# Optimization experiments

Measured on AMD Instinct MI355X. Metric: run time of the kernel, lower is better.

The kernel has to match this reference:

```python
import jax, jax.numpy as jnp
import numpy as np

H = 768          # hidden_size
NH = 12          # num heads
HD = H // NH     # head dim = 64
FF = 4 * H       # 3072
EPS = 1e-12


def _layer_norm(x, g, b):
    mu = jnp.mean(x, axis=-1, keepdims=True)
    var = jnp.var(x, axis=-1, keepdims=True)
    return (x - mu) * jax.lax.rsqrt(var + EPS) * g + b


def setup_inputs() -> dict:
    key = jax.random.key(0)
    ks = jax.random.split(key, 8)
    B, S = 4, 2048
    s = 0.02
    return {
        "x": jax.random.normal(ks[0], (B, S, H), dtype=jnp.float32),
        "w_qkv": jax.random.normal(ks[1], (H, 3 * H), dtype=jnp.float32) * s,
        "b_qkv": jnp.zeros((3 * H,), dtype=jnp.float32),
        "w_out": jax.random.normal(ks[2], (H, H), dtype=jnp.float32) * s,
        "b_out": jnp.zeros((H,), dtype=jnp.float32),
        "w_ff1": jax.random.normal(ks[3], (H, FF), dtype=jnp.float32) * s,
        "b_ff1": jnp.zeros((FF,), dtype=jnp.float32),
        "w_ff2": jax.random.normal(ks[4], (FF, H), dtype=jnp.float32) * s,
        "b_ff2": jnp.zeros((H,), dtype=jnp.float32),
        "g1": jnp.ones((H,), dtype=jnp.float32),
        "be1": jnp.zeros((H,), dtype=jnp.float32),
        "g2": jnp.ones((H,), dtype=jnp.float32),
        "be2": jnp.zeros((H,), dtype=jnp.float32),
    }


def reference(x, w_qkv, b_qkv, w_out, b_out, w_ff1, b_ff1, w_ff2, b_ff2, g1, be1, g2, be2):
    B, S, _ = x.shape
    qkv = x @ w_qkv + b_qkv                     # [B,S,3H]
    q, k, v = jnp.split(qkv, 3, axis=-1)
    # [B,S,H] -> [B,NH,S,HD]
    def heads(t):
        return t.reshape(B, S, NH, HD).transpose(0, 2, 1, 3)
    q, k, v = heads(q), heads(k), heads(v)
    scores = jnp.einsum("bhqd,bhkd->bhqk", q, k) / np.sqrt(HD).astype(np.float32)
    attn = jax.nn.softmax(scores, axis=-1)      # dropout is identity at inference
    ctx = jnp.einsum("bhqk,bhkd->bhqd", attn, v)
    ctx = ctx.transpose(0, 2, 1, 3).reshape(B, S, H)
    attn_out = ctx @ w_out + b_out
    x1 = _layer_norm(x + attn_out, g1, be1)
    h = jax.nn.gelu(x1 @ w_ff1 + b_ff1, approximate=False)  # torch exact gelu
    ffn = h @ w_ff2 + b_ff2
    return _layer_norm(x1 + ffn, g2, be2)
```

## Files before the change

### kernel.cpp

```cpp
#include <hip/hip_runtime.h>
#include <cstdint>
#include <cstddef>

typedef unsigned short u16;
typedef __attribute__((ext_vector_type(8))) short bf16x8;
typedef __attribute__((ext_vector_type(4))) float f32x4;
typedef __attribute__((ext_vector_type(16))) float f32x16;

__device__ __forceinline__ u16 f2b(float f) {
    union { float f; unsigned u; } un; un.f = f;
    unsigned r = un.u + 0x7fffu + ((un.u >> 16) & 1u);
    return (u16)(r >> 16);
}
__device__ __forceinline__ u16 f2b_trunc(float f) {
    union { float f; unsigned u; } un; un.f = f;
    return (u16)(un.u >> 16);
}
__device__ __forceinline__ float b2f(u16 h) {
    union { unsigned u; float f; } un; un.u = ((unsigned)h) << 16;
    return un.f;
}
__device__ __forceinline__ float fast_exp2(float x) {
#if __has_builtin(__builtin_amdgcn_exp2f)
    return __builtin_amdgcn_exp2f(x);
#else
    return exp2f(x);
#endif
}
__device__ __forceinline__ float fast_rcp(float x) {
#if __has_builtin(__builtin_amdgcn_rcpf)
    return __builtin_amdgcn_rcpf(x);
#else
    return 1.f / x;
#endif
}
__device__ __forceinline__ float gelu_fast(float v) {
    const float s = fast_exp2(v * (2.30220842f + 0.10294324f * (v * v)));
    return v - v * fast_rcp(s + 1.f);
}

__device__ __forceinline__ void stage16(const u16* g, u16* l) {
    __builtin_amdgcn_global_load_lds(
        (const __attribute__((address_space(1))) void*)g,
        (__attribute__((address_space(3))) void*)l, 16, 0, 0);
}

__global__ __launch_bounds__(256)
void prep(const float* __restrict__ x, u16* __restrict__ xb,
          const float* __restrict__ wqkv, u16* __restrict__ wqkvT,
          const float* __restrict__ wout, u16* __restrict__ woutT,
          const float* __restrict__ wff1, u16* __restrict__ wff1T,
          const float* __restrict__ wff2, u16* __restrict__ wff2T) {
    __shared__ float t[32][33];
    const int tid = threadIdx.x;
    int bid = blockIdx.x;
    if (bid < 6144) {
        const int i = bid * 256 + tid;
        float4 v = ((const float4*)x)[i];
        ushort4 o;
        o.x = f2b(v.x); o.y = f2b(v.y); o.z = f2b(v.z); o.w = f2b(v.w);
        ((ushort4*)xb)[i] = o;
        return;
    }
    int tt = bid - 6144;
    const float* in; u16* out; int K, N, bx, by;
    if (tt < 1728)      { in = wqkv; out = wqkvT; K = 768;  N = 2304; bx = tt % 72; by = tt / 72; }
    else if ((tt -= 1728) < 576)  { in = wout; out = woutT; K = 768;  N = 768;  bx = tt % 24; by = tt / 24; }
    else if ((tt -= 576) < 2304)  { in = wff1; out = wff1T; K = 768;  N = 3072; bx = tt % 96; by = tt / 96; }
    else { tt -= 2304;    in = wff2; out = wff2T; K = 3072; N = 768;  bx = tt % 24; by = tt / 24; }
    const int n0 = bx * 32, k0 = by * 32;
    const int tx = tid & 31, ty = tid >> 5;
#pragma unroll
    for (int i = 0; i < 4; ++i)
        t[ty + i * 8][tx] = in[(size_t)(k0 + ty + i * 8) * N + n0 + tx];
    __syncthreads();
#pragma unroll
    for (int i = 0; i < 4; ++i)
        out[(size_t)(n0 + ty + i * 8) * K + k0 + tx] = f2b(t[tx][ty + i * 8]);
}

template <int EPI, int NTW>
__global__ __launch_bounds__(256, 3)
void gemm_bf16(const u16* __restrict__ A, const u16* __restrict__ BT,
               const float* __restrict__ bias,
               void* __restrict__ outp, u16* __restrict__ vt, int M, int N, int K) {
    __shared__ __align__(16) u16 Ash[128 * 64];
    __shared__ __align__(16) u16 Bsh[NTW * 64 * 64];
    const int m0 = blockIdx.y * 128, n0 = blockIdx.x * (NTW * 64);
    const int tid = threadIdx.x;
    const int w = tid >> 6, lane = tid & 63;
    const int l32 = lane & 31, half = lane >> 5;
    const int wm = (w >> 1) * 64, wn = (w & 1) * (NTW * 32);

    const int srow = lane >> 3;
    const int sgrp = (lane & 7) ^ (srow & 7);
    const int xr = l32 & 7;

    f32x16 acc[2][NTW];
#pragma unroll
    for (int i = 0; i < 2; ++i)
#pragma unroll
        for (int j = 0; j < NTW; ++j)
#pragma unroll
            for (int e = 0; e < 16; ++e) acc[i][j][e] = 0.f;

    for (int k0 = 0; k0 < K; k0 += 64) {
#pragma unroll
        for (int it = 0; it < 4; ++it) {
            const int c = it * 4 + w;
            const int r = c * 8 + srow;
            stage16(A + (size_t)(m0 + r) * K + k0 + sgrp * 8, &Ash[c * 512 + lane * 8]);
        }
#pragma unroll
        for (int it = 0; it < 2 * NTW; ++it) {
            const int c = it * 4 + w;
            const int r = c * 8 + srow;
            stage16(BT + (size_t)(n0 + r) * K + k0 + sgrp * 8, &Bsh[c * 512 + lane * 8]);
        }
        __syncthreads();

        if constexpr (NTW == 2) {
            bf16x8 af[2][4], bfr[2][4];
#pragma unroll
            for (int mt = 0; mt < 2; ++mt)
#pragma unroll
                for (int kc = 0; kc < 4; ++kc)
                    af[mt][kc] = *(const bf16x8*)&Ash[(wm + mt * 32 + l32) * 64 +
                                                      (((kc << 1) + half) ^ xr) * 8];
#pragma unroll
            for (int nt = 0; nt < 2; ++nt)
#pragma unroll
                for (int kc = 0; kc < 4; ++kc)
                    bfr[nt][kc] = *(const bf16x8*)&Bsh[(wn + nt * 32 + l32) * 64 +
                                                       (((kc << 1) + half) ^ xr) * 8];
#pragma unroll
            for (int mt = 0; mt < 2; ++mt)
#pragma unroll
                for (int nt = 0; nt < 2; ++nt)
#pragma unroll
                    for (int kc = 0; kc < 4; ++kc)
                        acc[mt][nt] = __builtin_amdgcn_mfma_f32_32x32x16_bf16(
                            af[mt][kc], bfr[nt][kc], acc[mt][nt], 0, 0, 0);
        } else {
#pragma unroll
            for (int kc = 0; kc < 4; ++kc) {
                const int ko = (((kc << 1) + half) ^ xr) * 8;
                bf16x8 a0 = *(const bf16x8*)&Ash[(wm + l32) * 64 + ko];
                bf16x8 a1 = *(const bf16x8*)&Ash[(wm + 32 + l32) * 64 + ko];
#pragma unroll
                for (int nt = 0; nt < NTW; ++nt) {
                    bf16x8 bv = *(const bf16x8*)&Bsh[(wn + nt * 32 + l32) * 64 + ko];
                    acc[0][nt] = __builtin_amdgcn_mfma_f32_32x32x16_bf16(
                        a0, bv, acc[0][nt], 0, 0, 0);
                    acc[1][nt] = __builtin_amdgcn_mfma_f32_32x32x16_bf16(
                        a1, bv, acc[1][nt], 0, 0, 0);
                }
            }
        }
        __syncthreads();
    }

    if (EPI == 3 && n0 >= 1536) {
#pragma unroll
        for (int mt = 0; mt < 2; ++mt) {
#pragma unroll
            for (int nt = 0; nt < NTW; ++nt) {
                const int col = n0 + wn + nt * 32 + l32;
                const int c = col - 1536;
                const int h = c >> 6, d = c & 63;
                const float bv = bias[col];
#pragma unroll
                for (int rq = 0; rq < 4; ++rq) {
                    const int row0 = m0 + wm + mt * 32 + rq * 8 + half * 4;
                    const int b = row0 >> 11, tok = row0 & 2047;
                    ushort4 o;
                    o.x = f2b(acc[mt][nt][rq * 4 + 0] + bv);
                    o.y = f2b(acc[mt][nt][rq * 4 + 1] + bv);
                    o.z = f2b(acc[mt][nt][rq * 4 + 2] + bv);
                    o.w = f2b(acc[mt][nt][rq * 4 + 3] + bv);
                    *(ushort4*)&vt[(size_t)(((b * 12 + h) << 6) + d) * 2048 + tok] = o;
                }
            }
        }
        return;
    }

#pragma unroll
    for (int mt = 0; mt < 2; ++mt) {
#pragma unroll
        for (int nt = 0; nt < NTW; ++nt) {
            const int col = n0 + wn + nt * 32 + l32;
            const float bv = bias[col];
#pragma unroll
            for (int reg = 0; reg < 16; ++reg) {
                const int row = m0 + wm + mt * 32 + (reg & 3) + 8 * (reg >> 2) + 4 * half;
                float v = acc[mt][nt][reg] + bv;
                if (EPI == 2)
                    v = gelu_fast(v);
                ((u16*)outp)[(size_t)row * N + col] = f2b(v);
            }
        }
    }
}

template <bool RESF32>
__global__ __launch_bounds__(256, 4)
void gemm_bf16_r64(const u16* __restrict__ A, const u16* __restrict__ BT,
                   const float* __restrict__ bias, const void* __restrict__ resid,
                   u16* __restrict__ outp, int M, int N, int K) {
    __shared__ __align__(16) u16 Ash[64 * 64];
    __shared__ __align__(16) u16 Bsh[128 * 64];
    const int m0 = blockIdx.y * 64, n0 = blockIdx.x * 128;
    const int tid = threadIdx.x;
    const int w = tid >> 6, lane = tid & 63;
    const int l32 = lane & 31, half = lane >> 5;
    const int wm = (w >> 1) * 32, wn = (w & 1) * 64;

    const int srow = lane >> 3;
    const int sgrp = (lane & 7) ^ (srow & 7);
    const int xr = l32 & 7;

    f32x16 acc[2];
#pragma unroll
    for (int j = 0; j < 2; ++j)
#pragma unroll
        for (int e = 0; e < 16; ++e) acc[j][e] = 0.f;

    for (int k0 = 0; k0 < K; k0 += 64) {
#pragma unroll
        for (int it = 0; it < 2; ++it) {
            const int c = it * 4 + w;
            const int r = c * 8 + srow;
            stage16(A + (size_t)(m0 + r) * K + k0 + sgrp * 8, &Ash[c * 512 + lane * 8]);
        }
#pragma unroll
        for (int it = 0; it < 4; ++it) {
            const int c = it * 4 + w;
            const int r = c * 8 + srow;
            stage16(BT + (size_t)(n0 + r) * K + k0 + sgrp * 8, &Bsh[c * 512 + lane * 8]);
        }
        __syncthreads();

        bf16x8 af[4], bfr[2][4];
#pragma unroll
        for (int kc = 0; kc < 4; ++kc)
            af[kc] = *(const bf16x8*)&Ash[(wm + l32) * 64 + (((kc << 1) + half) ^ xr) * 8];
#pragma unroll
        for (int nt = 0; nt < 2; ++nt)
#pragma unroll
            for (int kc = 0; kc < 4; ++kc)
                bfr[nt][kc] = *(const bf16x8*)&Bsh[(wn + nt * 32 + l32) * 64 +
                                                   (((kc << 1) + half) ^ xr) * 8];
#pragma unroll
        for (int nt = 0; nt < 2; ++nt)
#pragma unroll
            for (int kc = 0; kc < 4; ++kc)
                acc[nt] = __builtin_amdgcn_mfma_f32_32x32x16_bf16(
                    af[kc], bfr[nt][kc], acc[nt], 0, 0, 0);
        __syncthreads();
    }

#pragma unroll
    for (int nt = 0; nt < 2; ++nt) {
        const int col = n0 + wn + nt * 32 + l32;
        const float bv = bias[col];
#pragma unroll
        for (int reg = 0; reg < 16; ++reg) {
            const int row = m0 + wm + (reg & 3) + 8 * (reg >> 2) + 4 * half;
            const size_t idx = (size_t)row * N + col;
            const float rv = RESF32 ? ((const float*)resid)[idx]
                                    : b2f(((const u16*)resid)[idx]);
            outp[idx] = f2b(acc[nt][reg] + bv + rv);
        }
    }
}

__global__ __launch_bounds__(256, 3)
void attn_fused(const u16* __restrict__ qkv, const u16* __restrict__ vt,
                u16* __restrict__ ctx) {
    constexpr int LDP = 68;
    __shared__ __align__(16) u16 Ksh[2][64 * 64];
    __shared__ __align__(16) u16 Vsh[2][64 * 64];
    __shared__ __align__(16) short Psh[4 * 32 * LDP];

    const int orig = blockIdx.x;
    const int swz = (orig & 7) * 96 + (orig >> 3);
    const int q0 = (swz & 15) * 128;
    const int bh = swz >> 4;
    const int h = bh % 12, b = bh / 12;

    const int tid = threadIdx.x;
    const int w = tid >> 6, lane = tid & 63, l16 = lane & 15, quad = lane >> 4;
    short* Pw = Psh + w * 32 * LDP;

    const int srow = lane >> 3;
    const int sgrp = (lane & 7) ^ (srow & 7);
    const int xk = l16 & 7;

    const u16* Qp = qkv + (size_t)b * 2048 * 2304 + h * 64;
    const u16* Kp = Qp + 768;
    const u16* Vtp = vt + ((size_t)(b * 12 + h) << 6) * 2048;

    bf16x8 qf[2][2];
#pragma unroll
    for (int mt = 0; mt < 2; ++mt)
#pragma unroll
        for (int s = 0; s < 2; ++s)
            qf[mt][s] = *(const bf16x8*)(Qp +
                (size_t)(q0 + w * 32 + mt * 16 + l16) * 2304 + s * 32 + quad * 8);
    asm volatile("s_waitcnt vmcnt(0)" ::: "memory");
    __builtin_amdgcn_sched_barrier(0);

    const f32x4 vzero = {0.f, 0.f, 0.f, 0.f};
    f32x4 oacc[2][4];
    float l_r[2][4];
#pragma unroll
    for (int mt = 0; mt < 2; ++mt) {
#pragma unroll
        for (int dt = 0; dt < 4; ++dt) oacc[mt][dt] = vzero;
#pragma unroll
        for (int r = 0; r < 4; ++r) l_r[mt][r] = 0.f;
    }

    constexpr float SCALE = 0.18033688011112042f;

    auto stage_kv = [&](int buf, int ktt) {
#pragma unroll
        for (int it = 0; it < 2; ++it) {
            const int c = it * 4 + w;
            const int r = c * 8 + srow;
            stage16(Kp + (size_t)(ktt + r) * 2304 + sgrp * 8,
                    &Ksh[buf][c * 512 + lane * 8]);
        }
#pragma unroll
        for (int it = 0; it < 2; ++it) {
            const int c = it * 4 + w;
            const int r = c * 8 + srow;
            stage16(Vtp + (size_t)r * 2048 + ktt + sgrp * 8,
                    &Vsh[buf][c * 512 + lane * 8]);
        }
    };

    stage_kv(0, 0);

    for (int t = 0; t < 32; ++t) {
        const int cur = t & 1;
        if (t < 31) {
            stage_kv(cur ^ 1, (t + 1) * 64);
            asm volatile("s_waitcnt vmcnt(4)" ::: "memory");
        } else {
            asm volatile("s_waitcnt vmcnt(0)" ::: "memory");
        }
        __builtin_amdgcn_sched_barrier(0);
        __builtin_amdgcn_s_barrier();

        bf16x8 kfr[4][2];
#pragma unroll
        for (int nt = 0; nt < 4; ++nt)
#pragma unroll
            for (int s = 0; s < 2; ++s)
                kfr[nt][s] = *(const bf16x8*)&Ksh[cur][(nt * 16 + l16) * 64 +
                                                      (((s << 2) + quad) ^ xk) * 8];

        f32x4 sacc[2][4];
        __builtin_amdgcn_s_setprio(1);
#pragma unroll
        for (int mt = 0; mt < 2; ++mt)
#pragma unroll
            for (int nt = 0; nt < 4; ++nt) {
                sacc[mt][nt] = vzero;
#pragma unroll
                for (int s = 0; s < 2; ++s)
                    sacc[mt][nt] = __builtin_amdgcn_mfma_f32_16x16x32_bf16(
                        qf[mt][s], kfr[nt][s], sacc[mt][nt], 0, 0, 0);
            }
        __builtin_amdgcn_s_setprio(0);

#pragma unroll
        for (int mt = 0; mt < 2; ++mt) {
#pragma unroll
            for (int r = 0; r < 4; ++r) {
                float p0 = fast_exp2(sacc[mt][0][r] * SCALE);
                float p1 = fast_exp2(sacc[mt][1][r] * SCALE);
                float p2 = fast_exp2(sacc[mt][2][r] * SCALE);
                float p3 = fast_exp2(sacc[mt][3][r] * SCALE);
                l_r[mt][r] += (p0 + p1) + (p2 + p3);
                short* prow = &Pw[(mt * 16 + quad * 4 + r) * LDP + l16];
                prow[0]  = (short)f2b_trunc(p0);
                prow[16] = (short)f2b_trunc(p1);
                prow[32] = (short)f2b_trunc(p2);
                prow[48] = (short)f2b_trunc(p3);
            }
        }

        bf16x8 vfr[4][2];
#pragma unroll
        for (int dt = 0; dt < 4; ++dt)
#pragma unroll
            for (int s = 0; s < 2; ++s)
                vfr[dt][s] = *(const bf16x8*)&Vsh[cur][(dt * 16 + l16) * 64 +
                                                      (((s << 2) + quad) ^ xk) * 8];

        __builtin_amdgcn_s_setprio(1);
#pragma unroll
        for (int mt = 0; mt < 2; ++mt) {
            bf16x8 pf[2];
#pragma unroll
            for (int s = 0; s < 2; ++s) {
                union { struct { short4 lo, hi; } h2; bf16x8 v; } u;
                const short* base = &Pw[(mt * 16 + l16) * LDP + s * 32 + quad * 8];
                u.h2.lo = *(const short4*)(base);
                u.h2.hi = *(const short4*)(base + 4);
                pf[s] = u.v;
            }
#pragma unroll
            for (int dt = 0; dt < 4; ++dt)
#pragma unroll
                for (int s = 0; s < 2; ++s)
                    oacc[mt][dt] = __builtin_amdgcn_mfma_f32_16x16x32_bf16(
                        pf[s], vfr[dt][s], oacc[mt][dt], 0, 0, 0);
        }
        __builtin_amdgcn_s_setprio(0);
        __builtin_amdgcn_s_barrier();
    }

#pragma unroll
    for (int mt = 0; mt < 2; ++mt)
#pragma unroll
        for (int r = 0; r < 4; ++r) {
#pragma unroll
            for (int off = 1; off < 16; off <<= 1)
                l_r[mt][r] += __shfl_xor(l_r[mt][r], off);
            l_r[mt][r] = 1.f / l_r[mt][r];
        }

#pragma unroll
    for (int mt = 0; mt < 2; ++mt)
#pragma unroll
        for (int dt = 0; dt < 4; ++dt)
#pragma unroll
            for (int r = 0; r < 4; ++r) {
                const int row = q0 + w * 32 + mt * 16 + quad * 4 + r;
                ctx[(size_t)(b * 2048 + row) * 768 + h * 64 + dt * 16 + l16] =
                    f2b(oacc[mt][dt][r] * l_r[mt][r]);
            }
}

template <bool OUTF32>
__global__ __launch_bounds__(256)
void layernorm_k(const u16* __restrict__ y, const float* __restrict__ g,
                 const float* __restrict__ be, float* __restrict__ outf,
                 u16* __restrict__ outb) {
    const int row = blockIdx.x;
    const int tid = threadIdx.x;
    const u16* yr = y + (size_t)row * 768;
    float v[3], s = 0.f, s2 = 0.f;
#pragma unroll
    for (int i = 0; i < 3; ++i) {
        float x = b2f(yr[tid + i * 256]);
        v[i] = x; s += x; s2 += x * x;
    }
#pragma unroll
    for (int off = 32; off >= 1; off >>= 1) {
        s += __shfl_xor(s, off);
        s2 += __shfl_xor(s2, off);
    }
    __shared__ float red[2][4];
    const int w = tid >> 6;
    if ((tid & 63) == 0) { red[0][w] = s; red[1][w] = s2; }
    __syncthreads();
    s = red[0][0] + red[0][1] + red[0][2] + red[0][3];
    s2 = red[1][0] + red[1][1] + red[1][2] + red[1][3];
    const float mu = s * (1.f / 768.f);
    const float var = s2 * (1.f / 768.f) - mu * mu;
    const float rs = rsqrtf(var + 1e-12f);
#pragma unroll
    for (int i = 0; i < 3; ++i) {
        const int c = tid + i * 256;
        const float o = (v[i] - mu) * rs * g[c] + be[c];
        if (OUTF32) outf[(size_t)row * 768 + c] = o;
        else        outb[(size_t)row * 768 + c] = f2b(o);
    }
}

extern "C" void kernel_launch(void* const* d_in, const int* in_sizes, int n_in,
                              void* d_out, int out_size, void* d_ws, size_t ws_size,
                              hipStream_t stream) {
    const float* x    = (const float*)d_in[0];
    const float* wqkv = (const float*)d_in[1];
    const float* bqkv = (const float*)d_in[2];
    const float* wout = (const float*)d_in[3];
    const float* bout = (const float*)d_in[4];
    const float* wff1 = (const float*)d_in[5];
    const float* bff1 = (const float*)d_in[6];
    const float* wff2 = (const float*)d_in[7];
    const float* bff2 = (const float*)d_in[8];
    const float* g1   = (const float*)d_in[9];
    const float* be1  = (const float*)d_in[10];
    const float* g2   = (const float*)d_in[11];
    const float* be2  = (const float*)d_in[12];

    char* ws = (char*)d_ws;
    constexpr size_t o_xb    = 0;
    constexpr size_t o_wqkvT = o_xb    + (size_t)8192 * 768 * 2;
    constexpr size_t o_woutT = o_wqkvT + (size_t)2304 * 768 * 2;
    constexpr size_t o_wff1T = o_woutT + (size_t)768 * 768 * 2;
    constexpr size_t o_wff2T = o_wff1T + (size_t)3072 * 768 * 2;
    constexpr size_t o_qkv   = o_wff2T + (size_t)768 * 3072 * 2;
    constexpr size_t o_ctx   = o_qkv   + (size_t)8192 * 2304 * 2;
    constexpr size_t o_y     = o_ctx   + (size_t)8192 * 768 * 2;
    constexpr size_t o_x1b   = o_y     + (size_t)8192 * 768 * 2;
    constexpr size_t o_vt    = o_x1b;
    constexpr size_t o_h     = o_qkv;

    u16*   xb    = (u16*)(ws + o_xb);
    u16*   wqkvT = (u16*)(ws + o_wqkvT);
    u16*   woutT = (u16*)(ws + o_woutT);
    u16*   wff1T = (u16*)(ws + o_wff1T);
    u16*   wff2T = (u16*)(ws + o_wff2T);
    u16*   qkvb  = (u16*)(ws + o_qkv);
    u16*   ctxb  = (u16*)(ws + o_ctx);
    u16*   yb    = (u16*)(ws + o_y);
    u16*   x1b   = (u16*)(ws + o_x1b);
    u16*   hb    = (u16*)(ws + o_h);
    u16*   vt    = (u16*)(ws + o_vt);

    prep<<<13056, 256, 0, stream>>>(x, xb, wqkv, wqkvT, wout, woutT,
                                    wff1, wff1T, wff2, wff2T);

    gemm_bf16<3, 3><<<dim3(2304 / 192, 8192 / 128), 256, 0, stream>>>(
        xb, wqkvT, bqkv, qkvb, vt, 8192, 2304, 768);

    attn_fused<<<768, 256, 0, stream>>>(qkvb, vt, ctxb);

    gemm_bf16_r64<true><<<dim3(768 / 128, 8192 / 64), 256, 0, stream>>>(
        ctxb, woutT, bout, x, yb, 8192, 768, 768);

    layernorm_k<false><<<8192, 256, 0, stream>>>(yb, g1, be1, nullptr, x1b);

    gemm_bf16<2, 2><<<dim3(3072 / 128, 8192 / 128), 256, 0, stream>>>(
        x1b, wff1T, bff1, hb, nullptr, 8192, 3072, 768);

    gemm_bf16_r64<false><<<dim3(768 / 128, 8192 / 64), 256, 0, stream>>>(
        hb, wff2T, bff2, x1b, yb, 8192, 768, 3072);

    layernorm_k<true><<<8192, 256, 0, stream>>>(yb, g2, be2, (float*)d_out, nullptr);
}
```

Before: 385.9 us.

## Use 32x32x16 MFMA with transposed S and in-register P via permlane swap

```diff
diff --git a/kernel.cpp b/kernel.cpp
--- a/kernel.cpp
+++ b/kernel.cpp
@@ -11,10 +11,6 @@
     union { float f; unsigned u; } un; un.f = f;
     unsigned r = un.u + 0x7fffu + ((un.u >> 16) & 1u);
     return (u16)(r >> 16);
-}
-__device__ __forceinline__ u16 f2b_trunc(float f) {
-    union { float f; unsigned u; } un; un.f = f;
-    return (u16)(un.u >> 16);
 }
 __device__ __forceinline__ float b2f(u16 h) {
     union { unsigned u; float f; } un; un.u = ((unsigned)h) << 16;
@@ -278,10 +274,8 @@
 __global__ __launch_bounds__(256, 3)
 void attn_fused(const u16* __restrict__ qkv, const u16* __restrict__ vt,
                 u16* __restrict__ ctx) {
-    constexpr int LDP = 68;
     __shared__ __align__(16) u16 Ksh[2][64 * 64];
     __shared__ __align__(16) u16 Vsh[2][64 * 64];
-    __shared__ __align__(16) short Psh[4 * 32 * LDP];
 
     const int orig = blockIdx.x;
     const int swz = (orig & 7) * 96 + (orig >> 3);
@@ -290,37 +284,31 @@
     const int h = bh % 12, b = bh / 12;
 
     const int tid = threadIdx.x;
-    const int w = tid >> 6, lane = tid & 63, l16 = lane & 15, quad = lane >> 4;
-    short* Pw = Psh + w * 32 * LDP;
+    const int w = tid >> 6, lane = tid & 63;
+    const int l32 = lane & 31, hi5 = lane >> 5;
+    const int xr8 = l32 & 7;
 
     const int srow = lane >> 3;
     const int sgrp = (lane & 7) ^ (srow & 7);
-    const int xk = l16 & 7;
 
     const u16* Qp = qkv + (size_t)b * 2048 * 2304 + h * 64;
     const u16* Kp = Qp + 768;
     const u16* Vtp = vt + ((size_t)(b * 12 + h) << 6) * 2048;
 
-    bf16x8 qf[2][2];
-#pragma unroll
-    for (int mt = 0; mt < 2; ++mt)
-#pragma unroll
-        for (int s = 0; s < 2; ++s)
-            qf[mt][s] = *(const bf16x8*)(Qp +
-                (size_t)(q0 + w * 32 + mt * 16 + l16) * 2304 + s * 32 + quad * 8);
+    bf16x8 qf[4];
+#pragma unroll
+    for (int ks = 0; ks < 4; ++ks)
+        qf[ks] = *(const bf16x8*)(Qp +
+            (size_t)(q0 + w * 32 + l32) * 2304 + ks * 16 + hi5 * 8);
     asm volatile("s_waitcnt vmcnt(0)" ::: "memory");
     __builtin_amdgcn_sched_barrier(0);
 
-    const f32x4 vzero = {0.f, 0.f, 0.f, 0.f};
-    f32x4 oacc[2][4];
-    float l_r[2][4];
-#pragma unroll
-    for (int mt = 0; mt < 2; ++mt) {
-#pragma unroll
-        for (int dt = 0; dt < 4; ++dt) oacc[mt][dt] = vzero;
-#pragma unroll
-        for (int r = 0; r < 4; ++r) l_r[mt][r] = 0.f;
-    }
+    f32x16 oacc[2];
+#pragma unroll
+    for (int dt = 0; dt < 2; ++dt)
+#pragma unroll
+        for (int e = 0; e < 16; ++e) oacc[dt][e] = 0.f;
+    float ls0 = 0.f, ls1 = 0.f, ls2 = 0.f, ls3 = 0.f;
 
     constexpr float SCALE = 0.18033688011112042f;
 
@@ -354,96 +342,91 @@
         __builtin_amdgcn_sched_barrier(0);
         __builtin_amdgcn_s_barrier();
 
-        bf16x8 kfr[4][2];
-#pragma unroll
-        for (int nt = 0; nt < 4; ++nt)
-#pragma unroll
-            for (int s = 0; s < 2; ++s)
-                kfr[nt][s] = *(const bf16x8*)&Ksh[cur][(nt * 16 + l16) * 64 +
-                                                      (((s << 2) + quad) ^ xk) * 8];
-
-        f32x4 sacc[2][4];
+        f32x16 sacc[2];
+#pragma unroll
+        for (int nt = 0; nt < 2; ++nt)
+#pragma unroll
+            for (int e = 0; e < 16; ++e) sacc[nt][e] = 0.f;
+
         __builtin_amdgcn_s_setprio(1);
 #pragma unroll
-        for (int mt = 0; mt < 2; ++mt)
-#pragma unroll
-            for (int nt = 0; nt < 4; ++nt) {
-                sacc[mt][nt] = vzero;
-#pragma unroll
-                for (int s = 0; s < 2; ++s)
-                    sacc[mt][nt] = __builtin_amdgcn_mfma_f32_16x16x32_bf16(
-                        qf[mt][s], kfr[nt][s], sacc[mt][nt], 0, 0, 0);
+        for (int nt = 0; nt < 2; ++nt)
+#pragma unroll
+            for (int ks = 0; ks < 4; ++ks) {
+                bf16x8 kfr = *(const bf16x8*)&Ksh[cur][(nt * 32 + l32) * 64 +
+                                                      (((ks << 1) + hi5) ^ xr8) * 8];
+                sacc[nt] = __builtin_amdgcn_mfma_f32_32x32x16_bf16(
+                    kfr, qf[ks], sacc[nt], 0, 0, 0);
             }
         __builtin_amdgcn_s_setprio(0);
 
 #pragma unroll
-        for (int mt = 0; mt < 2; ++mt) {
-#pragma unroll
-            for (int r = 0; r < 4; ++r) {
-                float p0 = fast_exp2(sacc[mt][0][r] * SCALE);
-                float p1 = fast_exp2(sacc[mt][1][r] * SCALE);
-                float p2 = fast_exp2(sacc[mt][2][r] * SCALE);
-                float p3 = fast_exp2(sacc[mt][3][r] * SCALE);
-                l_r[mt][r] += (p0 + p1) + (p2 + p3);
-                short* prow = &Pw[(mt * 16 + quad * 4 + r) * LDP + l16];
-                prow[0]  = (short)f2b_trunc(p0);
-                prow[16] = (short)f2b_trunc(p1);
-                prow[32] = (short)f2b_trunc(p2);
-                prow[48] = (short)f2b_trunc(p3);
+        for (int nt = 0; nt < 2; ++nt) {
+#pragma unroll
+            for (int e = 0; e < 16; ++e)
+                sacc[nt][e] = fast_exp2(sacc[nt][e] * SCALE);
+            ls0 += sacc[nt][0] + sacc[nt][1];
+            ls1 += sacc[nt][2] + sacc[nt][3];
+            ls2 += sacc[nt][4] + sacc[nt][5];
+            ls3 += sacc[nt][6] + sacc[nt][7];
+            ls0 += sacc[nt][8] + sacc[nt][9];
+            ls1 += sacc[nt][10] + sacc[nt][11];
+            ls2 += sacc[nt][12] + sacc[nt][13];
+            ls3 += sacc[nt][14] + sacc[nt][15];
+        }
+
+        __builtin_amdgcn_s_setprio(1);
+#pragma unroll
+        for (int nt = 0; nt < 2; ++nt) {
+#pragma unroll
+            for (int kh = 0; kh < 2; ++kh) {
+                const int rb = kh * 8;
+                unsigned c01, c23, c45, c67;
+                asm("v_cvt_pk_bf16_f32 %0, %1, %2"
+                    : "=v"(c01) : "v"(sacc[nt][rb + 0]), "v"(sacc[nt][rb + 1]));
+                asm("v_cvt_pk_bf16_f32 %0, %1, %2"
+                    : "=v"(c23) : "v"(sacc[nt][rb + 2]), "v"(sacc[nt][rb + 3]));
+                asm("v_cvt_pk_bf16_f32 %0, %1, %2"
+                    : "=v"(c45) : "v"(sacc[nt][rb + 4]), "v"(sacc[nt][rb + 5]));
+                asm("v_cvt_pk_bf16_f32 %0, %1, %2"
+                    : "=v"(c67) : "v"(sacc[nt][rb + 6]), "v"(sacc[nt][rb + 7]));
+                asm("v_permlane32_swap_b32 %0, %1" : "+v"(c01), "+v"(c45));
+                asm("v_permlane32_swap_b32 %0, %1" : "+v"(c23), "+v"(c67));
+                union { unsigned u[4]; bf16x8 v; } pf;
+                pf.u[0] = c01; pf.u[1] = c23; pf.u[2] = c45; pf.u[3] = c67;
+#pragma unroll
+                for (int dt = 0; dt < 2; ++dt) {
+                    bf16x8 vfr = *(const bf16x8*)&Vsh[cur][(dt * 32 + l32) * 64 +
+                        (((nt << 2) + (kh << 1) + hi5) ^ xr8) * 8];
+                    oacc[dt] = __builtin_amdgcn_mfma_f32_32x32x16_bf16(
+                        pf.v, vfr, oacc[dt], 0, 0, 0);
+                }
             }
-        }
-
-        bf16x8 vfr[4][2];
-#pragma unroll
-        for (int dt = 0; dt < 4; ++dt)
-#pragma unroll
-            for (int s = 0; s < 2; ++s)
-                vfr[dt][s] = *(const bf16x8*)&Vsh[cur][(dt * 16 + l16) * 64 +
-                                                      (((s << 2) + quad) ^ xk) * 8];
-
-        __builtin_amdgcn_s_setprio(1);
-#pragma unroll
-        for (int mt = 0; mt < 2; ++mt) {
-            bf16x8 pf[2];
-#pragma unroll
-            for (int s = 0; s < 2; ++s) {
-                union { struct { short4 lo, hi; } h2; bf16x8 v; } u;
-                const short* base = &Pw[(mt * 16 + l16) * LDP + s * 32 + quad * 8];
-                u.h2.lo = *(const short4*)(base);
-                u.h2.hi = *(const short4*)(base + 4);
-                pf[s] = u.v;
-            }
-#pragma unroll
-            for (int dt = 0; dt < 4; ++dt)
-#pragma unroll
-                for (int s = 0; s < 2; ++s)
-                    oacc[mt][dt] = __builtin_amdgcn_mfma_f32_16x16x32_bf16(
-                        pf[s], vfr[dt][s], oacc[mt][dt], 0, 0, 0);
         }
         __builtin_amdgcn_s_setprio(0);
         __builtin_amdgcn_s_barrier();
     }
 
-#pragma unroll
-    for (int mt = 0; mt < 2; ++mt)
-#pragma unroll
-        for (int r = 0; r < 4; ++r) {
-#pragma unroll
-            for (int off = 1; off < 16; off <<= 1)
-                l_r[mt][r] += __shfl_xor(l_r[mt][r], off);
-            l_r[mt][r] = 1.f / l_r[mt][r];
-        }
-
-#pragma unroll
-    for (int mt = 0; mt < 2; ++mt)
-#pragma unroll
-        for (int dt = 0; dt < 4; ++dt)
-#pragma unroll
-            for (int r = 0; r < 4; ++r) {
-                const int row = q0 + w * 32 + mt * 16 + quad * 4 + r;
-                ctx[(size_t)(b * 2048 + row) * 768 + h * 64 + dt * 16 + l16] =
-                    f2b(oacc[mt][dt][r] * l_r[mt][r]);
-            }
+    float lsum = (ls0 + ls1) + (ls2 + ls3);
+    lsum += __shfl_xor(lsum, 32);
+    const float linv = 1.f / lsum;
+
+    float scv[16];
+#pragma unroll
+    for (int reg = 0; reg < 16; ++reg) {
+        const int q_r = (reg & 3) + 8 * (reg >> 2) + 4 * hi5;
+        scv[reg] = __shfl(linv, q_r);
+    }
+
+#pragma unroll
+    for (int dt = 0; dt < 2; ++dt)
+#pragma unroll
+        for (int reg = 0; reg < 16; ++reg) {
+            const int q_r = (reg & 3) + 8 * (reg >> 2) + 4 * hi5;
+            const int row = q0 + w * 32 + q_r;
+            ctx[(size_t)(b * 2048 + row) * 768 + h * 64 + dt * 32 + l32] =
+                f2b(oacc[dt][reg] * scv[reg]);
+        }
 }
 
 template <bool OUTF32>
```

Result: faster. 367.6 us (-4.7%).
